# Performance work log

Measured on AMD Instinct MI355X. Metric: run time of the kernel, lower is better.

## Reference

```python
import jax, jax.numpy as jnp
import numpy as np

IDIM = 128
ODIM = 128
G = 8          # deformable groups
KH = KW = 3
K = KH * KW


def conv3x3(x, w, b):
    # x: [B,C,H,W], w: [O,I,3,3], stride 1, pad 1
    y = jax.lax.conv_general_dilated(x, w, (1, 1), ((1, 1), (1, 1)),
                                     dimension_numbers=('NCHW', 'OIHW', 'NCHW'))
    return y + b[None, :, None, None]


def deform_conv_v2(x, offset, mask, w, b):
    # x: [B,C,H,W]; offset: [B,2*G*K,H,W]; mask: [B,G*K,H,W] (pre-sigmoid)
    B, C, H, W = x.shape
    Cg = C // G
    off = offset.reshape(B, G, 2 * K, H, W)
    dy = off[:, :, 0::2]            # [B,G,K,H,W]
    dx = off[:, :, 1::2]
    m = jax.nn.sigmoid(mask).reshape(B, G, K, H, W)

    ky, kx = jnp.meshgrid(jnp.arange(KH), jnp.arange(KW), indexing='ij')
    ky = ky.reshape(K).astype(x.dtype)
    kx = kx.reshape(K).astype(x.dtype)
    hh = jnp.arange(H, dtype=x.dtype)
    ww = jnp.arange(W, dtype=x.dtype)
    # sampling positions (stride 1, pad 1, dilation 1)
    py = dy + (ky[:, None, None] + hh[None, :, None] - 1.0)   # [B,G,K,H,W]
    px = dx + (kx[:, None, None] + ww[None, None, :] - 1.0)

    y0 = jnp.floor(py)
    x0 = jnp.floor(px)
    ly = py - y0
    lx = px - x0

    x_flat = x.reshape(B, G, Cg, H * W)

    def gather(yi, xi):
        valid = ((yi >= 0) & (yi < H) & (xi >= 0) & (xi < W)).astype(x.dtype)
        yc = jnp.clip(yi, 0, H - 1).astype(jnp.int32)
        xc = jnp.clip(xi, 0, W - 1).astype(jnp.int32)
        idx = (yc * W + xc).reshape(B, G, 1, K * H * W)
        v = jnp.take_along_axis(x_flat, jnp.broadcast_to(idx, (B, G, Cg, K * H * W)), axis=3)
        return v.reshape(B, G, Cg, K, H, W) * valid[:, :, None]

    # bilinear interpolation with zero padding, fused with modulation mask
    v = (gather(y0, x0) * ((1 - ly) * (1 - lx))[:, :, None]
         + gather(y0, x0 + 1) * ((1 - ly) * lx)[:, :, None]
         + gather(y0 + 1, x0) * (ly * (1 - lx))[:, :, None]
         + gather(y0 + 1, x0 + 1) * (ly * lx)[:, :, None])
    v = v * m[:, :, None]                                      # [B,G,Cg,K,H,W]

    wr = w.reshape(w.shape[0], G, Cg, K)
    out = jnp.einsum('bgckhw,ogck->bohw', v, wr)
    return out + b[None, :, None, None]


def setup_inputs() -> dict:
    key = jax.random.key(0)
    ks = jax.random.split(key, 12)
    B, H, W = 2, 96, 96
    s = 0.05
    return {
        'R1': jax.random.normal(ks[0], (B, IDIM, H, W), jnp.float32),
        'Q0': jax.random.normal(ks[1], (B, IDIM, H, W), jnp.float32),
        'w1': jax.random.normal(ks[2], (ODIM, IDIM, 3, 3), jnp.float32) * s,
        'b1': jax.random.normal(ks[3], (ODIM,), jnp.float32) * s,
        'w2': jax.random.normal(ks[4], (ODIM, ODIM, 3, 3), jnp.float32) * s,
        'b2': jax.random.normal(ks[5], (ODIM,), jnp.float32) * s,
        'w_om': jax.random.normal(ks[6], (G * 3 * K, ODIM, 3, 3), jnp.float32) * s,
        'b_om': jax.random.normal(ks[7], (G * 3 * K,), jnp.float32) * s,
        'w_dcn': jax.random.normal(ks[8], (ODIM, IDIM, 3, 3), jnp.float32) * s,
        'b_dcn': jax.random.normal(ks[9], (ODIM,), jnp.float32) * s,
        'w_rq': jax.random.normal(ks[10], (ODIM, 2 * ODIM, 3, 3), jnp.float32) * s,
        'b_rq': jax.random.normal(ks[11], (ODIM,), jnp.float32) * s,
    }


def reference(R1, Q0, w1, b1, w2, b2, w_om, b_om, w_dcn, b_dcn, w_rq, b_rq):
    off = jax.nn.relu(conv3x3(R1 - Q0, w1, b1))
    off = jax.nn.relu(conv3x3(off, w2, b2))
    om = conv3x3(off, w_om, b_om)                 # [B, 3*G*K, H, W]
    o1, o2, mask = jnp.split(om, 3, axis=1)
    offset = jnp.concatenate([o1, o2], axis=1)    # [B, 2*G*K, H, W]
    fea = jax.nn.relu(deform_conv_v2(R1, offset, mask, w_dcn, b_dcn))
    fused = jnp.concatenate([fea, Q0], axis=1)
    return jax.nn.relu(conv3x3(fused, w_rq, b_rq))
```

## Files before the change

kernel.cpp:

```cpp
#include <hip/hip_runtime.h>

#define HH 96
#define WW 96
#define HW 9216
#define NPIX 18432
#define OMC 216
#define PP 9604

typedef __attribute__((ext_vector_type(8))) short short8x;
typedef __attribute__((ext_vector_type(8))) unsigned short ushort8x;
typedef __attribute__((ext_vector_type(4))) float f32x4;

__device__ __forceinline__ f32x4 mfma16(short8x a, short8x b, f32x4 c) {
    return __builtin_amdgcn_mfma_f32_16x16x32_bf16(a, b, c, 0, 0, 0);
}
__device__ __forceinline__ unsigned short f2bf(float f) {
    unsigned int u = __float_as_uint(f);
    u = (u + 0x7FFFu + ((u >> 16) & 1u)) >> 16;
    return (unsigned short)u;
}
__device__ __forceinline__ float bf2f(unsigned short b) {
    return __uint_as_float((unsigned int)b << 16);
}
__device__ __forceinline__ void split2(float v, unsigned short& h, unsigned short& l) {
    h = f2bf(v);
    l = f2bf(v - bf2f(h));
}
__device__ __forceinline__ void gld_lds16(const unsigned short* src, unsigned short* dst) {
    __builtin_amdgcn_global_load_lds(
        (const __attribute__((address_space(1))) unsigned int*)src,
        (__attribute__((address_space(3))) unsigned int*)dst, 16, 0, 0);
}

__global__ __launch_bounds__(256) void zero_borders(
    unsigned short* __restrict__ diffb,
    unsigned short* __restrict__ t1,
    unsigned short* __restrict__ catb)
{
    int idx = blockIdx.x * 256 + threadIdx.x;
    if (idx >= 99328) return;
    int i = idx >> 7, sub = idx & 127;
    int b = i / 388, r = i % 388;
    int y, x;
    if      (r < 98)  { y = 0;           x = r; }
    else if (r < 196) { y = 97;          x = r - 98; }
    else if (r < 292) { y = r - 196 + 1; x = 0; }
    else              { y = r - 292 + 1; x = 97; }
    size_t P = (size_t)b * PP + (size_t)y * 98 + x;
    ushort8x z = {};
    if (sub < 32)      *(ushort8x*)&diffb[P * 256 + sub * 8] = z;
    else if (sub < 64) *(ushort8x*)&t1[P * 256 + (sub - 32) * 8] = z;
    else               *(ushort8x*)&catb[P * 512 + (sub - 64) * 8] = z;
}

__global__ __launch_bounds__(256) void prep_acts(
    const float* __restrict__ R1, const float* __restrict__ Q0,
    unsigned short* __restrict__ r1b,
    unsigned short* __restrict__ diffb,
    unsigned short* __restrict__ cat)
{
    __shared__ float tR[128][64];
    __shared__ float tQ[128][64];
    int tid = threadIdx.x;
    int p0  = blockIdx.x * 64;
    int b   = p0 / HW;
    int rem0 = p0 % HW;

    for (int e = tid; e < 2048; e += 256) {
        int c = e >> 4, j = e & 15;
        size_t base = ((size_t)(b * 128 + c)) * HW + rem0;
        *(float4*)&tR[c][j * 4] = *(const float4*)(R1 + base + j * 4);
        *(float4*)&tQ[c][j * 4] = *(const float4*)(Q0 + base + j * 4);
    }
    __syncthreads();

    int p = tid & 63, half = tid >> 6;
    int c0 = half * 32;
    int pix = p0 + p;
    int rm = pix % HW, yy = rm / 96, xx = rm % 96;
    size_t P = (size_t)b * PP + (size_t)(yy + 1) * 98 + xx + 1;
    ushort8x rb[4], dh[4], dl[4], qh[4], ql[4];
    #pragma unroll
    for (int cc = 0; cc < 32; ++cc) {
        float r = tR[c0 + cc][p], q = tQ[c0 + cc][p];
        rb[cc >> 3][cc & 7] = f2bf(r);
        unsigned short h, l;
        split2(r - q, h, l); dh[cc >> 3][cc & 7] = h; dl[cc >> 3][cc & 7] = l;
        split2(q, h, l);     qh[cc >> 3][cc & 7] = h; ql[cc >> 3][cc & 7] = l;
    }
    #pragma unroll
    for (int i = 0; i < 4; ++i) {
        *(ushort8x*)&r1b[(size_t)pix * 128 + c0 + i * 8] = rb[i];
        *(ushort8x*)&diffb[P * 256 +       c0 + i * 8] = dh[i];
        *(ushort8x*)&diffb[P * 256 + 128 + c0 + i * 8] = dl[i];
        *(ushort8x*)&cat [P * 512 + 128 + c0 + i * 8] = qh[i];
        *(ushort8x*)&cat [P * 512 + 384 + c0 + i * 8] = ql[i];
    }
}

__global__ __launch_bounds__(256) void prep_w(
    const float* __restrict__ w1, const float* __restrict__ w2,
    const float* __restrict__ wom, const float* __restrict__ bom,
    const float* __restrict__ wrq, const float* __restrict__ wdcn,
    unsigned short* __restrict__ p1, unsigned short* __restrict__ p2,
    unsigned short* __restrict__ pom, unsigned short* __restrict__ prq,
    unsigned short* __restrict__ pdcn, float* __restrict__ bomp)
{
    int idx = blockIdx.x * 256 + threadIdx.x;
    unsigned short h, l;
    if (idx < 147456) {
        int t = idx / 16384, o = (idx >> 7) & 127, ci = idx & 127;
        int src = (o * 128 + ci) * 9 + t;
        split2(w1[src], h, l);  p1[idx] = h;  p1[idx + 147456] = l;
        split2(w2[src], h, l);  p2[idx] = h;  p2[idx + 147456] = l;
        int dd = o * 1152 + ((ci >> 4) * 9 + t) * 16 + (ci & 15);
        split2(wdcn[src], h, l); pdcn[dd] = h; pdcn[dd + 147456] = l;
    }
    if (idx < 294912) {
        {
            int t = idx / 32768, o = (idx >> 7) & 255, ci = idx & 127;
            float v = (o < OMC) ? wom[(o * 128 + ci) * 9 + t] : 0.f;
            split2(v, h, l); pom[idx] = h; pom[idx + 294912] = l;
        }
        {
            int t = idx / 32768, o = (idx >> 8) & 127, ci = idx & 255;
            split2(wrq[(o * 256 + ci) * 9 + t], h, l);
            prq[idx] = h; prq[idx + 294912] = l;
        }
    }
    if (idx < 256) bomp[idx] = (idx < OMC) ? bom[idx] : 0.f;
}

template<int CIN, int COUTP, int MODE, bool RELU>
__global__ __launch_bounds__(256, 2) void conv_mfma(
    const unsigned short* __restrict__ in,
    const unsigned short* __restrict__ wpk,
    const float* __restrict__ bias,
    void* __restrict__ outv)
{
    constexpr int NKC = CIN / 32;
    constexpr int NSTEP = 9 * NKC;
    const size_t WPLANE = (size_t)9 * COUTP * CIN;

    __shared__ __align__(16) unsigned short s_buf[3][3072 + 8192];

    int tid = threadIdx.x;
    int wid = tid >> 6, lane = tid & 63;
    int r = lane & 15, q = lane >> 4;
    int bid = blockIdx.x;
    int swz = (bid & 7) * 48 + (bid >> 3);
    int rowid = swz >> 1, half = swz & 1;
    int b = rowid / 96, y = rowid % 96;
    int x0 = half * 48;
    int nbase = blockIdx.y * 128;

    auto stage = [&](int buf, int step) {
        int t = step / NKC, kc = step - t * NKC;
        int dy = t / 3 - 1, dx = t % 3 - 1;
        unsigned short* sb = &s_buf[buf][0];
        {
            int j = tid;
            int m = j >> 7, pl = (j >> 6) & 1, L = j & 63;
            int px = m * 16 + (L & 15), qd = L >> 4;
            const unsigned short* src = in +
                ((size_t)b * PP + (size_t)(y + 1 + dy) * 98 + (x0 + 1 + dx + px)) * (2 * CIN)
                + pl * CIN + kc * 32 + qd * 8;
            gld_lds16(src, sb + (size_t)(wid * 64) * 8);
        }
        if (tid < 128) {
            int j = 256 + tid;
            int m = j >> 7, pl = (j >> 6) & 1, L = j & 63;
            int px = m * 16 + (L & 15), qd = L >> 4;
            const unsigned short* src = in +
                ((size_t)b * PP + (size_t)(y + 1 + dy) * 98 + (x0 + 1 + dx + px)) * (2 * CIN)
                + pl * CIN + kc * 32 + qd * 8;
            gld_lds16(src, sb + (size_t)(256 + wid * 64) * 8);
        }
        const unsigned short* wbase = wpk + ((size_t)t * COUTP + nbase) * CIN + kc * 32;
        #pragma unroll
        for (int c = 0; c < 4; ++c) {
            int j = c * 256 + tid;
            int ni = (j >> 7) & 1, pl = (j >> 6) & 1, L = j & 63;
            int rr = L & 15, qq = L >> 4;
            const unsigned short* src = wbase + (size_t)pl * WPLANE
                + (size_t)(c * 32 + ni * 16 + rr) * CIN + qq * 8;
            gld_lds16(src, sb + 3072 + (size_t)(c * 256 + wid * 64) * 8);
        }
    };

    f32x4 acc[3][2] = {};

    auto compute = [&](int buf) {
        const unsigned short* sb = &s_buf[buf][0];
        short8x AH[3], AL[3], BH[2], BL[2];
        #pragma unroll
        for (int m = 0; m < 3; ++m) {
            AH[m] = *(const short8x*)(sb + m * 1024 + lane * 8);
            AL[m] = *(const short8x*)(sb + m * 1024 + 512 + lane * 8);
        }
        #pragma unroll
        for (int n = 0; n < 2; ++n) {
            BH[n] = *(const short8x*)(sb + 3072 + wid * 2048 + n * 1024 + lane * 8);
            BL[n] = *(const short8x*)(sb + 3072 + wid * 2048 + n * 1024 + 512 + lane * 8);
        }
        #pragma unroll
        for (int m = 0; m < 3; ++m) {
            #pragma unroll
            for (int n = 0; n < 2; ++n) {
                acc[m][n] = mfma16(AH[m], BH[n], acc[m][n]);
                acc[m][n] = mfma16(AL[m], BH[n], acc[m][n]);
                acc[m][n] = mfma16(AH[m], BL[n], acc[m][n]);
            }
        }
    };

    stage(0, 0);
    stage(1, 1);
    if (tid < 128) asm volatile("s_waitcnt vmcnt(6)" ::: "memory");
    else           asm volatile("s_waitcnt vmcnt(5)" ::: "memory");
    __builtin_amdgcn_s_barrier();

    for (int k = 0; k < NSTEP; ++k) {
        const int nb = k + 2;
        if (nb < NSTEP) stage(nb % 3, nb);
        compute(k % 3);
        if (k + 1 < NSTEP) {
            if (nb < NSTEP) {
                if (tid < 128) asm volatile("s_waitcnt vmcnt(6)" ::: "memory");
                else           asm volatile("s_waitcnt vmcnt(5)" ::: "memory");
            } else {
                asm volatile("s_waitcnt vmcnt(0)" ::: "memory");
            }
            __builtin_amdgcn_s_barrier();
        }
    }

    #pragma unroll
    for (int m = 0; m < 3; ++m) {
        #pragma unroll
        for (int n = 0; n < 2; ++n) {
            int o = nbase + wid * 32 + n * 16 + r;
            float bv = bias[o];
            #pragma unroll
            for (int j = 0; j < 4; ++j) {
                int px = m * 16 + q * 4 + j;
                int xx = x0 + px;
                float v = acc[m][n][j] + bv;
                if (RELU) v = fmaxf(v, 0.f);
                if (MODE == 0) {
                    size_t P = (size_t)b * PP + (size_t)(y + 1) * 98 + xx + 1;
                    unsigned short h, l; split2(v, h, l);
                    ((unsigned short*)outv)[P * 2 * COUTP + o] = h;
                    ((unsigned short*)outv)[P * 2 * COUTP + COUTP + o] = l;
                } else if (MODE == 1) {
                    if (o < OMC)
                        ((unsigned short*)outv)[((size_t)b * HW + y * 96 + xx) * OMC + o] = f2bf(v);
                } else {
                    ((float*)outv)[((size_t)b * 128 + o) * HW + y * 96 + xx] = v;
                }
            }
        }
    }
}

__global__ __launch_bounds__(256, 3) void deform_mfma(
    const unsigned short* __restrict__ xb,
    const unsigned short* __restrict__ omf,
    const unsigned short* __restrict__ wpk,
    const float* __restrict__ bias,
    unsigned short* __restrict__ cat)
{
    __shared__ __align__(16) unsigned short s_v[16][1160];
    __shared__ __align__(16) unsigned short s_om[16][216];

    int tid = threadIdx.x;
    int bid = blockIdx.x;
    int swzb = (bid & 7) * 144 + (bid >> 3);
    int pix0 = swzb * 16;
    int b = pix0 / HW;

    for (int it = tid; it < 432; it += 256) {
        int p = it / 27, j = it - p * 27;
        *(ushort8x*)&s_om[p][j * 8] =
            *(const ushort8x*)&omf[(size_t)(pix0 + p) * OMC + j * 8];
    }
    __syncthreads();

    for (int e = tid; e < 1152; e += 256) {
        int p = e & 15, gk = e >> 4;
        int pix = pix0 + p;
        int rem = pix % HW;
        int hh = rem / 96, ww = rem % 96;
        int g = gk / 9, k = gk % 9;
        const unsigned short* op = &s_om[p][0];
        float dy = bf2f(op[g * 18 + 2 * k]);
        float dx = bf2f(op[g * 18 + 2 * k + 1]);
        float mr = bf2f(op[144 + g * 9 + k]);
        float m = 1.f / (1.f + __expf(-mr));
        float py = dy + (float)(k / 3) + (float)hh - 1.f;
        float px = dx + (float)(k % 3) + (float)ww - 1.f;
        float fy = floorf(py), fx = floorf(px);
        int y0 = (int)fy, x0 = (int)fx;
        float ly = py - fy, lx = px - fx;
        float cw[4] = {(1.f - ly) * (1.f - lx), (1.f - ly) * lx,
                       ly * (1.f - lx), ly * lx};
        ushort8x cv0[4], cv1[4];
        #pragma unroll
        for (int j = 0; j < 4; ++j) {
            int yy = y0 + (j >> 1), xx = x0 + (j & 1);
            bool valid = ((unsigned)yy < 96u) && ((unsigned)xx < 96u);
            int yc = min(max(yy, 0), 95), xc = min(max(xx, 0), 95);
            const unsigned short* cp =
                xb + ((size_t)(b * HW + yc * 96 + xc)) * 128 + g * 16;
            cv0[j] = *(const ushort8x*)cp;
            cv1[j] = *(const ushort8x*)(cp + 8);
            cw[j] = valid ? cw[j] * m : 0.f;
        }
        ushort8x o0, o1;
        #pragma unroll
        for (int i = 0; i < 8; ++i) {
            float v0 = cw[0] * bf2f(cv0[0][i]) + cw[1] * bf2f(cv0[1][i])
                     + cw[2] * bf2f(cv0[2][i]) + cw[3] * bf2f(cv0[3][i]);
            float v1 = cw[0] * bf2f(cv1[0][i]) + cw[1] * bf2f(cv1[1][i])
                     + cw[2] * bf2f(cv1[2][i]) + cw[3] * bf2f(cv1[3][i]);
            o0[i] = f2bf(v0);
            o1[i] = f2bf(v1);
        }
        *(ushort8x*)&s_v[p][gk * 16    ] = o0;
        *(ushort8x*)&s_v[p][gk * 16 + 8] = o1;
    }
    __syncthreads();

    int wid = tid >> 6, lane = tid & 63;
    int r = lane & 15, q = lane >> 4;
    int n0 = wid * 32;
    f32x4 acc0 = {}, acc1 = {};
    const unsigned short* wb = wpk + (size_t)(n0 + r) * 1152 + q * 8;
    __builtin_amdgcn_s_setprio(1);
    #pragma unroll
    for (int kp = 0; kp < 18; ++kp) {
        const int k0 = kp * 2, k1 = k0 + 1;
        short8x a0 = *(const short8x*)&s_v[r][k0 * 32 + q * 8];
        short8x a1 = *(const short8x*)&s_v[r][k1 * 32 + q * 8];
        short8x w00 = *(const short8x*)(wb + k0 * 32);
        short8x w10 = *(const short8x*)(wb + (size_t)16 * 1152 + k0 * 32);
        short8x l00 = *(const short8x*)(wb + 147456 + k0 * 32);
        short8x l10 = *(const short8x*)(wb + 147456 + (size_t)16 * 1152 + k0 * 32);
        short8x w01 = *(const short8x*)(wb + k1 * 32);
        short8x w11 = *(const short8x*)(wb + (size_t)16 * 1152 + k1 * 32);
        short8x l01 = *(const short8x*)(wb + 147456 + k1 * 32);
        short8x l11 = *(const short8x*)(wb + 147456 + (size_t)16 * 1152 + k1 * 32);
        acc0 = mfma16(a0, w00, acc0);
        acc1 = mfma16(a0, w10, acc1);
        acc0 = mfma16(a0, l00, acc0);
        acc1 = mfma16(a0, l10, acc1);
        acc0 = mfma16(a1, w01, acc0);
        acc1 = mfma16(a1, w11, acc1);
        acc0 = mfma16(a1, l01, acc0);
        acc1 = mfma16(a1, l11, acc1);
    }
    __builtin_amdgcn_s_setprio(0);
    #pragma unroll
    for (int ni = 0; ni < 2; ++ni) {
        f32x4 A = ni ? acc1 : acc0;
        int o = n0 + ni * 16 + r;
        float bv = bias[o];
        #pragma unroll
        for (int j = 0; j < 4; ++j) {
            int pixel = pix0 + q * 4 + j;
            int bb = pixel / HW, rm = pixel % HW;
            int yy = rm / 96, xx = rm % 96;
            size_t P = (size_t)bb * PP + (size_t)(yy + 1) * 98 + xx + 1;
            float v = fmaxf(A[j] + bv, 0.f);
            unsigned short h, l;
            split2(v, h, l);
            cat[P * 512 + o] = h;
            cat[P * 512 + 256 + o] = l;
        }
    }
}

extern "C" void kernel_launch(void* const* d_in, const int* in_sizes, int n_in,
                              void* d_out, int out_size, void* d_ws, size_t ws_size,
                              hipStream_t stream) {
    const float* R1    = (const float*)d_in[0];
    const float* Q0    = (const float*)d_in[1];
    const float* w1    = (const float*)d_in[2];
    const float* b1    = (const float*)d_in[3];
    const float* w2    = (const float*)d_in[4];
    const float* b2    = (const float*)d_in[5];
    const float* w_om  = (const float*)d_in[6];
    const float* b_om  = (const float*)d_in[7];
    const float* w_dcn = (const float*)d_in[8];
    const float* b_dcn = (const float*)d_in[9];
    const float* w_rq  = (const float*)d_in[10];
    const float* b_rq  = (const float*)d_in[11];
    float* outp = (float*)d_out;

    char* w = (char*)d_ws;
    unsigned short* r1b   = (unsigned short*)w; w += (size_t)NPIX * 128 * 2;
    unsigned short* diffb = (unsigned short*)w; w += (size_t)2 * PP * 256 * 2;
    unsigned short* t1    = (unsigned short*)w; w += (size_t)2 * PP * 256 * 2;
    unsigned short* catb  = (unsigned short*)w; w += (size_t)2 * PP * 512 * 2;
    unsigned short* p1    = (unsigned short*)w; w += 2 * 147456 * 2;
    unsigned short* p2    = (unsigned short*)w; w += 2 * 147456 * 2;
    unsigned short* pdcn  = (unsigned short*)w; w += 2 * 147456 * 2;
    unsigned short* pom   = (unsigned short*)w; w += 2 * 294912 * 2;
    unsigned short* prq   = (unsigned short*)w; w += 2 * 294912 * 2;
    float*          bomp  = (float*)w;          w += 256 * 4;
    unsigned short* t2    = diffb;
    unsigned short* omf   = t1;

    zero_borders<<<388, 256, 0, stream>>>(diffb, t1, catb);
    prep_acts<<<288, 256, 0, stream>>>(R1, Q0, r1b, diffb, catb);
    prep_w<<<1152, 256, 0, stream>>>(w1, w2, w_om, b_om, w_rq, w_dcn,
                                     p1, p2, pom, prq, pdcn, bomp);

    conv_mfma<128, 128, 0, true ><<<dim3(384, 1), 256, 0, stream>>>(diffb, p1, b1, t1);
    conv_mfma<128, 128, 0, true ><<<dim3(384, 1), 256, 0, stream>>>(t1,    p2, b2, t2);
    conv_mfma<128, 256, 1, false><<<dim3(384, 2), 256, 0, stream>>>(t2,   pom, bomp, omf);

    deform_mfma<<<1152, 256, 0, stream>>>(r1b, omf, pdcn, b_dcn, catb);

    conv_mfma<256, 128, 2, true ><<<dim3(384, 1), 256, 0, stream>>>(catb, prq, b_rq, outp);
}
```

Baseline: 388.4 us.

## Split deform sampling into two halves and overlap gather loads with MFMA

The deformable sampling buffer is split into two K-halves. The first half is sampled and stored, then the corner loads for the second half are issued before the MFMA pass over the first half, so gather latency hides behind matrix math. The second half is finished and its MFMA pass runs after a barrier. This holds many more vector registers live across the MFMA loop, which could hurt occupancy at the launch bound of 3 blocks and cause spills.

```diff
diff --git a/kernel.cpp b/kernel.cpp
--- a/kernel.cpp
+++ b/kernel.cpp
@@ -270,7 +270,7 @@
     const float* __restrict__ bias,
     unsigned short* __restrict__ cat)
 {
-    __shared__ __align__(16) unsigned short s_v[16][1160];
+    __shared__ __align__(16) unsigned short s_v[2][16][584];
     __shared__ __align__(16) unsigned short s_om[16][216];
 
     int tid = threadIdx.x;
@@ -286,12 +286,14 @@
     }
     __syncthreads();
 
-    for (int e = tid; e < 1152; e += 256) {
-        int p = e & 15, gk = e >> 4;
+    auto prep = [&](int hf, int e, ushort8x (&c0)[4], ushort8x (&c1)[4],
+                    float (&cw)[4], int& pp, int& gl) {
+        int p = e & 15, gkl = e >> 4;
+        int gk = hf * 36 + gkl;
         int pix = pix0 + p;
         int rem = pix % HW;
         int hh = rem / 96, ww = rem % 96;
-        int g = gk / 9, k = gk % 9;
+        int g = gk / 9, k = gk - g * 9;
         const unsigned short* op = &s_om[p][0];
         float dy = bf2f(op[g * 18 + 2 * k]);
         float dx = bf2f(op[g * 18 + 2 * k + 1]);
@@ -302,9 +304,8 @@
         float fy = floorf(py), fx = floorf(px);
         int y0 = (int)fy, x0 = (int)fx;
         float ly = py - fy, lx = px - fx;
-        float cw[4] = {(1.f - ly) * (1.f - lx), (1.f - ly) * lx,
+        float wj[4] = {(1.f - ly) * (1.f - lx), (1.f - ly) * lx,
                        ly * (1.f - lx), ly * lx};
-        ushort8x cv0[4], cv1[4];
         #pragma unroll
         for (int j = 0; j < 4; ++j) {
             int yy = y0 + (j >> 1), xx = x0 + (j & 1);
@@ -312,22 +313,32 @@
             int yc = min(max(yy, 0), 95), xc = min(max(xx, 0), 95);
             const unsigned short* cp =
                 xb + ((size_t)(b * HW + yc * 96 + xc)) * 128 + g * 16;
-            cv0[j] = *(const ushort8x*)cp;
-            cv1[j] = *(const ushort8x*)(cp + 8);
-            cw[j] = valid ? cw[j] * m : 0.f;
-        }
+            c0[j] = *(const ushort8x*)cp;
+            c1[j] = *(const ushort8x*)(cp + 8);
+            cw[j] = valid ? wj[j] * m : 0.f;
+        }
+        pp = p; gl = gkl;
+    };
+    auto finish = [&](int hf, ushort8x (&c0)[4], ushort8x (&c1)[4],
+                      float (&cw)[4], int pp, int gl) {
         ushort8x o0, o1;
         #pragma unroll
         for (int i = 0; i < 8; ++i) {
-            float v0 = cw[0] * bf2f(cv0[0][i]) + cw[1] * bf2f(cv0[1][i])
-                     + cw[2] * bf2f(cv0[2][i]) + cw[3] * bf2f(cv0[3][i]);
-            float v1 = cw[0] * bf2f(cv1[0][i]) + cw[1] * bf2f(cv1[1][i])
-                     + cw[2] * bf2f(cv1[2][i]) + cw[3] * bf2f(cv1[3][i]);
+            float v0 = cw[0]*bf2f(c0[0][i]) + cw[1]*bf2f(c0[1][i])
+                     + cw[2]*bf2f(c0[2][i]) + cw[3]*bf2f(c0[3][i]);
+            float v1 = cw[0]*bf2f(c1[0][i]) + cw[1]*bf2f(c1[1][i])
+                     + cw[2]*bf2f(c1[2][i]) + cw[3]*bf2f(c1[3][i]);
             o0[i] = f2bf(v0);
             o1[i] = f2bf(v1);
         }
-        *(ushort8x*)&s_v[p][gk * 16    ] = o0;
-        *(ushort8x*)&s_v[p][gk * 16 + 8] = o1;
+        *(ushort8x*)&s_v[hf][pp][gl * 16    ] = o0;
+        *(ushort8x*)&s_v[hf][pp][gl * 16 + 8] = o1;
+    };
+
+    for (int e = tid; e < 576; e += 256) {
+        ushort8x c0[4], c1[4]; float cw[4]; int pp, gl;
+        prep(0, e, c0, c1, cw, pp, gl);
+        finish(0, c0, c1, cw, pp, gl);
     }
     __syncthreads();
 
@@ -336,30 +347,52 @@
     int n0 = wid * 32;
     f32x4 acc0 = {}, acc1 = {};
     const unsigned short* wb = wpk + (size_t)(n0 + r) * 1152 + q * 8;
-    __builtin_amdgcn_s_setprio(1);
-    #pragma unroll
-    for (int kp = 0; kp < 18; ++kp) {
-        const int k0 = kp * 2, k1 = k0 + 1;
-        short8x a0 = *(const short8x*)&s_v[r][k0 * 32 + q * 8];
-        short8x a1 = *(const short8x*)&s_v[r][k1 * 32 + q * 8];
-        short8x w00 = *(const short8x*)(wb + k0 * 32);
-        short8x w10 = *(const short8x*)(wb + (size_t)16 * 1152 + k0 * 32);
-        short8x l00 = *(const short8x*)(wb + 147456 + k0 * 32);
-        short8x l10 = *(const short8x*)(wb + 147456 + (size_t)16 * 1152 + k0 * 32);
-        short8x w01 = *(const short8x*)(wb + k1 * 32);
-        short8x w11 = *(const short8x*)(wb + (size_t)16 * 1152 + k1 * 32);
-        short8x l01 = *(const short8x*)(wb + 147456 + k1 * 32);
-        short8x l11 = *(const short8x*)(wb + 147456 + (size_t)16 * 1152 + k1 * 32);
-        acc0 = mfma16(a0, w00, acc0);
-        acc1 = mfma16(a0, w10, acc1);
-        acc0 = mfma16(a0, l00, acc0);
-        acc1 = mfma16(a0, l10, acc1);
-        acc0 = mfma16(a1, w01, acc0);
-        acc1 = mfma16(a1, w11, acc1);
-        acc0 = mfma16(a1, l01, acc0);
-        acc1 = mfma16(a1, l11, acc1);
-    }
-    __builtin_amdgcn_s_setprio(0);
+
+    auto phaseC = [&](int hf) {
+        __builtin_amdgcn_s_setprio(1);
+        #pragma unroll
+        for (int kpl = 0; kpl < 9; ++kpl) {
+            const int k0 = hf * 18 + kpl * 2, k1 = k0 + 1;
+            short8x a0 = *(const short8x*)&s_v[hf][r][kpl * 64 + q * 8];
+            short8x a1 = *(const short8x*)&s_v[hf][r][kpl * 64 + 32 + q * 8];
+            short8x w00 = *(const short8x*)(wb + k0 * 32);
+            short8x w10 = *(const short8x*)(wb + (size_t)16 * 1152 + k0 * 32);
+            short8x l00 = *(const short8x*)(wb + 147456 + k0 * 32);
+            short8x l10 = *(const short8x*)(wb + 147456 + (size_t)16 * 1152 + k0 * 32);
+            short8x w01 = *(const short8x*)(wb + k1 * 32);
+            short8x w11 = *(const short8x*)(wb + (size_t)16 * 1152 + k1 * 32);
+            short8x l01 = *(const short8x*)(wb + 147456 + k1 * 32);
+            short8x l11 = *(const short8x*)(wb + 147456 + (size_t)16 * 1152 + k1 * 32);
+            acc0 = mfma16(a0, w00, acc0);
+            acc1 = mfma16(a0, w10, acc1);
+            acc0 = mfma16(a0, l00, acc0);
+            acc1 = mfma16(a0, l10, acc1);
+            acc0 = mfma16(a1, w01, acc0);
+            acc1 = mfma16(a1, w11, acc1);
+            acc0 = mfma16(a1, l01, acc0);
+            acc1 = mfma16(a1, l11, acc1);
+        }
+        __builtin_amdgcn_s_setprio(0);
+    };
+
+    ushort8x Ac0[4], Ac1[4]; float Acw[4]; int Ap, Agl;
+    ushort8x Bc0[4], Bc1[4]; float Bcw[4]; int Bp, Bgl;
+    prep(1, tid,       Ac0, Ac1, Acw, Ap, Agl);
+    prep(1, tid + 256, Bc0, Bc1, Bcw, Bp, Bgl);
+    asm volatile("" ::: "memory");
+
+    phaseC(0);
+
+    finish(1, Ac0, Ac1, Acw, Ap, Agl);
+    finish(1, Bc0, Bc1, Bcw, Bp, Bgl);
+    if (tid < 64) {
+        prep(1, tid + 512, Ac0, Ac1, Acw, Ap, Agl);
+        finish(1, Ac0, Ac1, Acw, Ap, Agl);
+    }
+    __syncthreads();
+
+    phaseC(1);
+
     #pragma unroll
     for (int ni = 0; ni < 2; ++ni) {
         f32x4 A = ni ? acc1 : acc0;
```

Measured after the change: 387.9 us, median of 3. No clear change (-0.1%).

## Process 32 pixels per deform block, splitting K into two halves for weight reuse

Applied to the files above, without the earlier changes.

The deformable conv kernel now handles 32 pixels per block instead of 16 and launches half as many blocks. The K dimension is split into two halves, so the sampled-value tile in shared memory stays the same size. Each weight fragment loaded from global memory is reused across two 16-pixel MFMA tiles, which halves weight traffic per pixel. In exchange there is an extra barrier between the halves, more accumulator registers, and fewer blocks to fill the GPU.

```diff
diff --git a/kernel.cpp b/kernel.cpp
--- a/kernel.cpp
+++ b/kernel.cpp
@@ -270,112 +270,124 @@
     const float* __restrict__ bias,
     unsigned short* __restrict__ cat)
 {
-    __shared__ __align__(16) unsigned short s_v[16][1160];
-    __shared__ __align__(16) unsigned short s_om[16][216];
+    __shared__ __align__(16) unsigned short s_v[32][584];
+    __shared__ __align__(16) unsigned short s_om[32][216];
 
     int tid = threadIdx.x;
     int bid = blockIdx.x;
-    int swzb = (bid & 7) * 144 + (bid >> 3);
-    int pix0 = swzb * 16;
+    int swzb = (bid & 7) * 72 + (bid >> 3);
+    int pix0 = swzb * 32;
     int b = pix0 / HW;
 
-    for (int it = tid; it < 432; it += 256) {
+    for (int it = tid; it < 864; it += 256) {
         int p = it / 27, j = it - p * 27;
         *(ushort8x*)&s_om[p][j * 8] =
             *(const ushort8x*)&omf[(size_t)(pix0 + p) * OMC + j * 8];
     }
     __syncthreads();
 
-    for (int e = tid; e < 1152; e += 256) {
-        int p = e & 15, gk = e >> 4;
-        int pix = pix0 + p;
-        int rem = pix % HW;
-        int hh = rem / 96, ww = rem % 96;
-        int g = gk / 9, k = gk % 9;
-        const unsigned short* op = &s_om[p][0];
-        float dy = bf2f(op[g * 18 + 2 * k]);
-        float dx = bf2f(op[g * 18 + 2 * k + 1]);
-        float mr = bf2f(op[144 + g * 9 + k]);
-        float m = 1.f / (1.f + __expf(-mr));
-        float py = dy + (float)(k / 3) + (float)hh - 1.f;
-        float px = dx + (float)(k % 3) + (float)ww - 1.f;
-        float fy = floorf(py), fx = floorf(px);
-        int y0 = (int)fy, x0 = (int)fx;
-        float ly = py - fy, lx = px - fx;
-        float cw[4] = {(1.f - ly) * (1.f - lx), (1.f - ly) * lx,
-                       ly * (1.f - lx), ly * lx};
-        ushort8x cv0[4], cv1[4];
-        #pragma unroll
-        for (int j = 0; j < 4; ++j) {
-            int yy = y0 + (j >> 1), xx = x0 + (j & 1);
-            bool valid = ((unsigned)yy < 96u) && ((unsigned)xx < 96u);
-            int yc = min(max(yy, 0), 95), xc = min(max(xx, 0), 95);
-            const unsigned short* cp =
-                xb + ((size_t)(b * HW + yc * 96 + xc)) * 128 + g * 16;
-            cv0[j] = *(const ushort8x*)cp;
-            cv1[j] = *(const ushort8x*)(cp + 8);
-            cw[j] = valid ? cw[j] * m : 0.f;
-        }
-        ushort8x o0, o1;
-        #pragma unroll
-        for (int i = 0; i < 8; ++i) {
-            float v0 = cw[0] * bf2f(cv0[0][i]) + cw[1] * bf2f(cv0[1][i])
-                     + cw[2] * bf2f(cv0[2][i]) + cw[3] * bf2f(cv0[3][i]);
-            float v1 = cw[0] * bf2f(cv1[0][i]) + cw[1] * bf2f(cv1[1][i])
-                     + cw[2] * bf2f(cv1[2][i]) + cw[3] * bf2f(cv1[3][i]);
-            o0[i] = f2bf(v0);
-            o1[i] = f2bf(v1);
-        }
-        *(ushort8x*)&s_v[p][gk * 16    ] = o0;
-        *(ushort8x*)&s_v[p][gk * 16 + 8] = o1;
-    }
-    __syncthreads();
-
     int wid = tid >> 6, lane = tid & 63;
     int r = lane & 15, q = lane >> 4;
     int n0 = wid * 32;
-    f32x4 acc0 = {}, acc1 = {};
+    f32x4 acc[2][2] = {};
     const unsigned short* wb = wpk + (size_t)(n0 + r) * 1152 + q * 8;
-    __builtin_amdgcn_s_setprio(1);
+
     #pragma unroll
-    for (int kp = 0; kp < 18; ++kp) {
-        const int k0 = kp * 2, k1 = k0 + 1;
-        short8x a0 = *(const short8x*)&s_v[r][k0 * 32 + q * 8];
-        short8x a1 = *(const short8x*)&s_v[r][k1 * 32 + q * 8];
-        short8x w00 = *(const short8x*)(wb + k0 * 32);
-        short8x w10 = *(const short8x*)(wb + (size_t)16 * 1152 + k0 * 32);
-        short8x l00 = *(const short8x*)(wb + 147456 + k0 * 32);
-        short8x l10 = *(const short8x*)(wb + 147456 + (size_t)16 * 1152 + k0 * 32);
-        short8x w01 = *(const short8x*)(wb + k1 * 32);
-        short8x w11 = *(const short8x*)(wb + (size_t)16 * 1152 + k1 * 32);
-        short8x l01 = *(const short8x*)(wb + 147456 + k1 * 32);
-        short8x l11 = *(const short8x*)(wb + 147456 + (size_t)16 * 1152 + k1 * 32);
-        acc0 = mfma16(a0, w00, acc0);
-        acc1 = mfma16(a0, w10, acc1);
-        acc0 = mfma16(a0, l00, acc0);
-        acc1 = mfma16(a0, l10, acc1);
-        acc0 = mfma16(a1, w01, acc0);
-        acc1 = mfma16(a1, w11, acc1);
-        acc0 = mfma16(a1, l01, acc0);
-        acc1 = mfma16(a1, l11, acc1);
-    }
-    __builtin_amdgcn_s_setprio(0);
+    for (int hf = 0; hf < 2; ++hf) {
+        for (int e = tid; e < 1152; e += 256) {
+            int p = e & 31, gkl = e >> 5;
+            int gk = hf * 36 + gkl;
+            int pix = pix0 + p;
+            int rem = pix % HW;
+            int hh = rem / 96, ww = rem % 96;
+            int g = gk / 9, k = gk - g * 9;
+            const unsigned short* op = &s_om[p][0];
+            float dy = bf2f(op[g * 18 + 2 * k]);
+            float dx = bf2f(op[g * 18 + 2 * k + 1]);
+            float mr = bf2f(op[144 + g * 9 + k]);
+            float m = 1.f / (1.f + __expf(-mr));
+            float py = dy + (float)(k / 3) + (float)hh - 1.f;
+            float px = dx + (float)(k % 3) + (float)ww - 1.f;
+            float fy = floorf(py), fx = floorf(px);
+            int y0 = (int)fy, x0 = (int)fx;
+            float ly = py - fy, lx = px - fx;
+            float cw[4] = {(1.f - ly) * (1.f - lx), (1.f - ly) * lx,
+                           ly * (1.f - lx), ly * lx};
+            ushort8x cv0[4], cv1[4];
+            #pragma unroll
+            for (int j = 0; j < 4; ++j) {
+                int yy = y0 + (j >> 1), xx = x0 + (j & 1);
+                bool valid = ((unsigned)yy < 96u) && ((unsigned)xx < 96u);
+                int yc = min(max(yy, 0), 95), xc = min(max(xx, 0), 95);
+                const unsigned short* cp =
+                    xb + ((size_t)(b * HW + yc * 96 + xc)) * 128 + g * 16;
+                cv0[j] = *(const ushort8x*)cp;
+                cv1[j] = *(const ushort8x*)(cp + 8);
+                cw[j] = valid ? cw[j] * m : 0.f;
+            }
+            ushort8x o0, o1;
+            #pragma unroll
+            for (int i = 0; i < 8; ++i) {
+                float v0 = cw[0] * bf2f(cv0[0][i]) + cw[1] * bf2f(cv0[1][i])
+                         + cw[2] * bf2f(cv0[2][i]) + cw[3] * bf2f(cv0[3][i]);
+                float v1 = cw[0] * bf2f(cv1[0][i]) + cw[1] * bf2f(cv1[1][i])
+                         + cw[2] * bf2f(cv1[2][i]) + cw[3] * bf2f(cv1[3][i]);
+                o0[i] = f2bf(v0);
+                o1[i] = f2bf(v1);
+            }
+            *(ushort8x*)&s_v[p][gkl * 16    ] = o0;
+            *(ushort8x*)&s_v[p][gkl * 16 + 8] = o1;
+        }
+        __syncthreads();
+
+        __builtin_amdgcn_s_setprio(1);
+        #pragma unroll
+        for (int kpl = 0; kpl < 9; ++kpl) {
+            const int k0 = hf * 18 + kpl * 2, k1 = k0 + 1;
+            short8x w00 = *(const short8x*)(wb + k0 * 32);
+            short8x w10 = *(const short8x*)(wb + (size_t)16 * 1152 + k0 * 32);
+            short8x l00 = *(const short8x*)(wb + 147456 + k0 * 32);
+            short8x l10 = *(const short8x*)(wb + 147456 + (size_t)16 * 1152 + k0 * 32);
+            short8x w01 = *(const short8x*)(wb + k1 * 32);
+            short8x w11 = *(const short8x*)(wb + (size_t)16 * 1152 + k1 * 32);
+            short8x l01 = *(const short8x*)(wb + 147456 + k1 * 32);
+            short8x l11 = *(const short8x*)(wb + 147456 + (size_t)16 * 1152 + k1 * 32);
+            #pragma unroll
+            for (int m = 0; m < 2; ++m) {
+                short8x a0 = *(const short8x*)&s_v[m * 16 + r][kpl * 64 + q * 8];
+                short8x a1 = *(const short8x*)&s_v[m * 16 + r][kpl * 64 + 32 + q * 8];
+                acc[m][0] = mfma16(a0, w00, acc[m][0]);
+                acc[m][1] = mfma16(a0, w10, acc[m][1]);
+                acc[m][0] = mfma16(a0, l00, acc[m][0]);
+                acc[m][1] = mfma16(a0, l10, acc[m][1]);
+                acc[m][0] = mfma16(a1, w01, acc[m][0]);
+                acc[m][1] = mfma16(a1, w11, acc[m][1]);
+                acc[m][0] = mfma16(a1, l01, acc[m][0]);
+                acc[m][1] = mfma16(a1, l11, acc[m][1]);
+            }
+        }
+        __builtin_amdgcn_s_setprio(0);
+        if (hf == 0) __syncthreads();
+    }
+
     #pragma unroll
-    for (int ni = 0; ni < 2; ++ni) {
-        f32x4 A = ni ? acc1 : acc0;
-        int o = n0 + ni * 16 + r;
-        float bv = bias[o];
-        #pragma unroll
-        for (int j = 0; j < 4; ++j) {
-            int pixel = pix0 + q * 4 + j;
-            int bb = pixel / HW, rm = pixel % HW;
-            int yy = rm / 96, xx = rm % 96;
-            size_t P = (size_t)bb * PP + (size_t)(yy + 1) * 98 + xx + 1;
-            float v = fmaxf(A[j] + bv, 0.f);
-            unsigned short h, l;
-            split2(v, h, l);
-            cat[P * 512 + o] = h;
-            cat[P * 512 + 256 + o] = l;
+    for (int m = 0; m < 2; ++m) {
+        #pragma unroll
+        for (int ni = 0; ni < 2; ++ni) {
+            int o = n0 + ni * 16 + r;
+            float bv = bias[o];
+            #pragma unroll
+            for (int j = 0; j < 4; ++j) {
+                int pixel = pix0 + m * 16 + q * 4 + j;
+                int bb = pixel / HW, rm = pixel % HW;
+                int yy = rm / 96, xx = rm % 96;
+                size_t P = (size_t)bb * PP + (size_t)(yy + 1) * 98 + xx + 1;
+                float v = fmaxf(acc[m][ni][j] + bv, 0.f);
+                unsigned short h, l;
+                split2(v, h, l);
+                cat[P * 512 + o] = h;
+                cat[P * 512 + 256 + o] = l;
+            }
         }
     }
 }
@@ -420,7 +432,7 @@
     conv_mfma<128, 128, 0, true ><<<dim3(384, 1), 256, 0, stream>>>(t1,    p2, b2, t2);
     conv_mfma<128, 256, 1, false><<<dim3(384, 2), 256, 0, stream>>>(t2,   pom, bomp, omf);
 
-    deform_mfma<<<1152, 256, 0, stream>>>(r1b, omf, pdcn, b_dcn, catb);
+    deform_mfma<<<576, 256, 0, stream>>>(r1b, omf, pdcn, b_dcn, catb);
 
     conv_mfma<256, 128, 2, true ><<<dim3(384, 1), 256, 0, stream>>>(catb, prq, b_rq, outp);
 }
```

New measurement: 360.8 us, median of 2. -7.1%, faster.
